# Performance work log

Hardware: AMD Instinct MI355X
Metric: run time of the kernel (lower is better)

Reference implementation:

```python
import jax, jax.numpy as jnp
import numpy as np

N = 100000   # nodes
DIM = 128    # feature dim
E = 800000   # edges per hop
K = 4        # hops
BN_EPS = 1e-5


def setup_inputs() -> dict:
    key = jax.random.key(0)
    ks = jax.random.split(key, 24)
    inp = {}
    for i in range(K):
        inp[f"x{i}"] = jax.random.normal(ks[i], (N, DIM), dtype=jnp.float32)
    inp["edge_attr"] = jax.random.normal(ks[4], (E, DIM), dtype=jnp.float32)
    for i in range(K):
        inp[f"e{i}"] = jax.random.randint(ks[5 + i], (2, E), 0, N, dtype=jnp.int32)
    s1 = 1.0 / np.sqrt(DIM)
    s2 = 1.0 / np.sqrt(2 * DIM)
    inp["W1"] = jax.random.uniform(ks[9], (DIM, 2 * DIM), jnp.float32, -s1, s1)
    inp["b1"] = jax.random.uniform(ks[10], (2 * DIM,), jnp.float32, -s1, s1)
    inp["bn1_g"] = jnp.ones((2 * DIM,), jnp.float32)
    inp["bn1_b"] = jnp.zeros((2 * DIM,), jnp.float32)
    inp["W2"] = jax.random.uniform(ks[11], (2 * DIM, DIM), jnp.float32, -s2, s2)
    inp["b2"] = jax.random.uniform(ks[12], (DIM,), jnp.float32, -s2, s2)
    inp["bn2_g"] = jnp.ones((DIM,), jnp.float32)
    inp["bn2_b"] = jnp.zeros((DIM,), jnp.float32)
    inp["bn3_g"] = jnp.ones((DIM,), jnp.float32)
    inp["bn3_b"] = jnp.zeros((DIM,), jnp.float32)
    inp["eps_param"] = jnp.zeros((K + 1, DIM), jnp.float32)  # nn.Parameter(zeros)
    return inp


def _bn(h, g, b):
    # BatchNorm1d, train-mode math: batch mean / biased var per feature
    m = jnp.mean(h, axis=0)
    v = jnp.var(h, axis=0)
    return g * (h - m) * jax.lax.rsqrt(v + BN_EPS) + b


def _propagate(x, edge_index, edge_attr):
    # message: relu(x_j [+ edge_attr]); aggregate: scatter-add at dst
    msg = x[edge_index[0]]                      # [E, DIM] gather from src
    if edge_attr is not None:
        msg = msg + edge_attr
    msg = jax.nn.relu(msg)
    return jax.ops.segment_sum(msg, edge_index[1], num_segments=N)


def reference(x0, x1, x2, x3, edge_attr, e0, e1, e2, e3,
              W1, b1, bn1_g, bn1_b, W2, b2, bn2_g, bn2_b,
              bn3_g, bn3_b, eps_param):
    xs = [x0, x1, x2, x3]
    es = [e0, e1, e2, e3]
    result = (1.0 + eps_param[0]) * x0
    for i in range(K):
        ea = edge_attr if i == 0 else None
        result = result + (1.0 + eps_param[i + 1]) * _propagate(xs[i], es[i], ea)
    # GIN MLP: Linear -> BN -> ReLU -> Linear -> BN -> ReLU
    h = jax.nn.relu(_bn(result @ W1 + b1, bn1_g, bn1_b))
    h = jax.nn.relu(_bn(h @ W2 + b2, bn2_g, bn2_b))
    # outer ConvBlock: BN -> act (relu, not last layer); dropout in eval = identity
    h = jax.nn.relu(_bn(h, bn3_g, bn3_b))
    return h  # new x[0]; original also carries XX through unchanged
```

## Files before the change

kernel.cpp:

```cpp
#include <hip/hip_runtime.h>
#include <cstdint>
#include <cstddef>

#define NN 100000
#define D 128
#define NE 800000
#define BN_EPS 1e-5f

#define M4 (4 * NN)
#define CH 1000
#define NB 400
#define GB 782

typedef __attribute__((ext_vector_type(4))) float f32x4;
typedef __attribute__((ext_vector_type(2))) float f32x2;
typedef __attribute__((ext_vector_type(8))) short s16x8;

__device__ inline unsigned short f2bf(float f) {
  unsigned int u = __builtin_bit_cast(unsigned int, f);
  u += 0x7FFFu + ((u >> 16) & 1u);
  return (unsigned short)(u >> 16);
}
__device__ inline float bf2f(unsigned short u) {
  unsigned int x = ((unsigned int)u) << 16;
  return __builtin_bit_cast(float, x);
}
__device__ inline f32x2 ntload2(const float* p) {
  return __builtin_nontemporal_load(reinterpret_cast<const f32x2*>(p));
}

__global__ __launch_bounds__(256) void k_prep(const float* __restrict__ W1,
                                              const float* __restrict__ W2,
                                              unsigned short* __restrict__ W1T,
                                              unsigned short* __restrict__ W2T) {
  int i = blockIdx.x * 256 + threadIdx.x;
  if (i >= 32768) return;
  int k1 = i >> 8, n1 = i & 255;
  W1T[n1 * 128 + k1] = f2bf(W1[i]);
  int k2 = i >> 7, n2 = i & 127;
  W2T[n2 * 256 + k2] = f2bf(W2[i]);
}

__global__ __launch_bounds__(256) void k_count(
    const int* __restrict__ e0, const int* __restrict__ e1,
    const int* __restrict__ e2, const int* __restrict__ e3,
    unsigned int* __restrict__ pcount, unsigned char* __restrict__ wrank) {
  const int h = blockIdx.y;
  const int* e = h == 0 ? e0 : h == 1 ? e1 : h == 2 ? e2 : e3;
  const int eid = blockIdx.x * 256 + threadIdx.x;
  const int dst = e[NE + eid];
  unsigned int old = atomicAdd(&pcount[dst], 1u << (8 * h));
  wrank[h * NE + eid] = (unsigned char)((old >> (8 * h)) & 0xFFu);
}

__global__ __launch_bounds__(256) void k_scanA(const unsigned int* __restrict__ pcount,
                                               int* __restrict__ bsum) {
  __shared__ int red[256];
  const int b = blockIdx.x, t = threadIdx.x;
  int s = 0;
  if (t < 250) {
    unsigned int p = pcount[b * 250 + t];
    s = (int)((p & 0xFFu) + ((p >> 8) & 0xFFu) + ((p >> 16) & 0xFFu) + (p >> 24));
  }
  red[t] = s; __syncthreads();
  for (int off = 128; off > 0; off >>= 1) {
    if (t < off) red[t] += red[t + off];
    __syncthreads();
  }
  if (t == 0) bsum[b] = red[0];
}

__global__ __launch_bounds__(512) void k_scanB(const int* __restrict__ bsum,
                                               int* __restrict__ bpre) {
  __shared__ int s[512];
  const int t = threadIdx.x;
  const int v = (t < NB) ? bsum[t] : 0;
  s[t] = v; __syncthreads();
  for (int off = 1; off < 512; off <<= 1) {
    int x = s[t];
    if (t >= off) x += s[t - off];
    __syncthreads(); s[t] = x; __syncthreads();
  }
  if (t < NB) bpre[t] = s[t] - v;
}

__global__ __launch_bounds__(256) void k_scanC(const unsigned int* __restrict__ pcount,
                                               const int* __restrict__ bpre,
                                               int* __restrict__ offsets) {
  __shared__ int cnt[CH];
  __shared__ int part[256];
  const int b = blockIdx.x, t = threadIdx.x;
  if (t < 250) {
    unsigned int p = pcount[b * 250 + t];
    cnt[t * 4 + 0] = (int)(p & 0xFFu);
    cnt[t * 4 + 1] = (int)((p >> 8) & 0xFFu);
    cnt[t * 4 + 2] = (int)((p >> 16) & 0xFFu);
    cnt[t * 4 + 3] = (int)(p >> 24);
  }
  __syncthreads();
  int own = 0;
#pragma unroll
  for (int j = 0; j < 4; j++) {
    int idx = t * 4 + j;
    if (idx < CH) own += cnt[idx];
  }
  part[t] = own; __syncthreads();
  for (int off = 1; off < 256; off <<= 1) {
    int x = part[t];
    if (t >= off) x += part[t - off];
    __syncthreads(); part[t] = x; __syncthreads();
  }
  int run = bpre[b] + part[t] - own;
#pragma unroll
  for (int j = 0; j < 4; j++) {
    int idx = t * 4 + j;
    if (idx < CH) { offsets[b * CH + idx] = run; run += cnt[idx]; }
  }
  if (b == 0 && t == 0) offsets[M4] = 4 * NE;
}

__global__ __launch_bounds__(256) void k_place(
    const int* __restrict__ e0, const int* __restrict__ e1,
    const int* __restrict__ e2, const int* __restrict__ e3,
    const int* __restrict__ offsets, const unsigned char* __restrict__ wrank,
    int* __restrict__ srcs, int* __restrict__ eids) {
  const int h = blockIdx.y;
  const int* e = h == 0 ? e0 : h == 1 ? e1 : h == 2 ? e2 : e3;
  const int eid = blockIdx.x * 256 + threadIdx.x;
  const int dst = e[NE + eid];
  const int pos = offsets[dst * 4 + h] + (int)wrank[h * NE + eid];
  if (h == 0) {
    eids[pos] = eid;
  } else {
    srcs[pos] = e[eid];
  }
}

__global__ __launch_bounds__(256) void k_gather(
    const float* __restrict__ x0, const float* __restrict__ x1,
    const float* __restrict__ x2, const float* __restrict__ x3,
    const float* __restrict__ edge_attr, const float* __restrict__ eps,
    const int* __restrict__ e0, const int* __restrict__ offsets,
    const int* __restrict__ srcs, const int* __restrict__ eids,
    unsigned short* __restrict__ result) {
  const int dst  = blockIdx.x * 4 + (threadIdx.x >> 6);
  const int lane = threadIdx.x & 63;
  const int d    = lane * 2;

  const int4 ob = *reinterpret_cast<const int4*>(offsets + 4 * dst);
  const int o0 = ob.x, b1 = ob.y, b2 = ob.z, b3 = ob.w;
  const int o4 = offsets[4 * dst + 4];

  float2 h0 = make_float2(0.f, 0.f);
  float2 h1 = make_float2(0.f, 0.f);
  float2 h2 = make_float2(0.f, 0.f);
  float2 h3 = make_float2(0.f, 0.f);

  {
    int j = o0;
    for (; j + 4 <= b1; j += 4) {
      const int q0 = eids[j], q1 = eids[j + 1], q2 = eids[j + 2], q3 = eids[j + 3];
      const int p0 = e0[q0], p1 = e0[q1], p2 = e0[q2], p3 = e0[q3];
      f32x2 w0 = ntload2(edge_attr + (size_t)q0 * D + d);
      f32x2 w1 = ntload2(edge_attr + (size_t)q1 * D + d);
      f32x2 w2 = ntload2(edge_attr + (size_t)q2 * D + d);
      f32x2 w3 = ntload2(edge_attr + (size_t)q3 * D + d);
      float2 v0 = *reinterpret_cast<const float2*>(x0 + p0 * D + d);
      float2 v1 = *reinterpret_cast<const float2*>(x0 + p1 * D + d);
      float2 v2 = *reinterpret_cast<const float2*>(x0 + p2 * D + d);
      float2 v3 = *reinterpret_cast<const float2*>(x0 + p3 * D + d);
      h0.x += fmaxf(v0.x + w0[0], 0.f); h0.y += fmaxf(v0.y + w0[1], 0.f);
      h0.x += fmaxf(v1.x + w1[0], 0.f); h0.y += fmaxf(v1.y + w1[1], 0.f);
      h0.x += fmaxf(v2.x + w2[0], 0.f); h0.y += fmaxf(v2.y + w2[1], 0.f);
      h0.x += fmaxf(v3.x + w3[0], 0.f); h0.y += fmaxf(v3.y + w3[1], 0.f);
    }
    for (; j < b1; ++j) {
      const int q = eids[j];
      const int p = e0[q];
      f32x2 w = ntload2(edge_attr + (size_t)q * D + d);
      float2 v = *reinterpret_cast<const float2*>(x0 + p * D + d);
      h0.x += fmaxf(v.x + w[0], 0.f); h0.y += fmaxf(v.y + w[1], 0.f);
    }
  }

#define HOP_LOOP(XP, ACC, BEG, END) do {                                       \
    int j_ = (BEG);                                                            \
    for (; j_ + 4 <= (END); j_ += 4) {                                         \
      const int p0_ = srcs[j_], p1_ = srcs[j_ + 1];                            \
      const int p2_ = srcs[j_ + 2], p3_ = srcs[j_ + 3];                        \
      float2 v0_ = *reinterpret_cast<const float2*>((XP) + p0_ * D + d);       \
      float2 v1_ = *reinterpret_cast<const float2*>((XP) + p1_ * D + d);       \
      float2 v2_ = *reinterpret_cast<const float2*>((XP) + p2_ * D + d);       \
      float2 v3_ = *reinterpret_cast<const float2*>((XP) + p3_ * D + d);       \
      ACC.x += fmaxf(v0_.x, 0.f); ACC.y += fmaxf(v0_.y, 0.f);                  \
      ACC.x += fmaxf(v1_.x, 0.f); ACC.y += fmaxf(v1_.y, 0.f);                  \
      ACC.x += fmaxf(v2_.x, 0.f); ACC.y += fmaxf(v2_.y, 0.f);                  \
      ACC.x += fmaxf(v3_.x, 0.f); ACC.y += fmaxf(v3_.y, 0.f);                  \
    }                                                                          \
    for (; j_ < (END); ++j_) {                                                 \
      const int p_ = srcs[j_];                                                 \
      float2 v_ = *reinterpret_cast<const float2*>((XP) + p_ * D + d);         \
      ACC.x += fmaxf(v_.x, 0.f); ACC.y += fmaxf(v_.y, 0.f);                    \
    }                                                                          \
  } while (0)

  HOP_LOOP(x1, h1, b1, b2);
  HOP_LOOP(x2, h2, b2, b3);
  HOP_LOOP(x3, h3, b3, o4);
#undef HOP_LOOP

  float2 e0v = *reinterpret_cast<const float2*>(eps + d);
  float2 s1 = *reinterpret_cast<const float2*>(eps + 1 * D + d);
  float2 s2 = *reinterpret_cast<const float2*>(eps + 2 * D + d);
  float2 s3 = *reinterpret_cast<const float2*>(eps + 3 * D + d);
  float2 s4 = *reinterpret_cast<const float2*>(eps + 4 * D + d);
  float2 xv = *reinterpret_cast<const float2*>(x0 + dst * D + d);

  float ax = (1.f + e0v.x) * xv.x + (1.f + s1.x) * h0.x + (1.f + s2.x) * h1.x
           + (1.f + s3.x) * h2.x + (1.f + s4.x) * h3.x;
  float ay = (1.f + e0v.y) * xv.y + (1.f + s1.y) * h0.y + (1.f + s2.y) * h1.y
           + (1.f + s3.y) * h2.y + (1.f + s4.y) * h3.y;

  reinterpret_cast<unsigned int*>(result)[dst * 64 + lane] =
      (unsigned int)f2bf(ax) | ((unsigned int)f2bf(ay) << 16);
}

__global__ __launch_bounds__(512) void k_gemm1(const unsigned short* __restrict__ Ab,
                                               const unsigned short* __restrict__ W1T,
                                               unsigned short* __restrict__ t1b,
                                               float* __restrict__ sums1,
                                               float* __restrict__ sumsq1) {
  __shared__ float ls[256], lq[256];
  const int tid = threadIdx.x;
  if (tid < 256) { ls[tid] = 0.f; lq[tid] = 0.f; }
  __syncthreads();

  const int lane = tid & 63, wave = tid >> 6;
  const int ln = lane & 15, lk = lane >> 4;
  const int m0 = blockIdx.x * 128 + wave * 16;
  const int arow = m0 + ln;
  const bool av = arow < NN;

  f32x4 acc[16];
#pragma unroll
  for (int t = 0; t < 16; t++) acc[t] = (f32x4)0.f;

#pragma unroll
  for (int kk = 0; kk < 4; kk++) {
    const int kb = kk * 32 + lk * 8;
    s16x8 a = (s16x8)(short)0;
    if (av) a = *reinterpret_cast<const s16x8*>(Ab + arow * 128 + kb);
#pragma unroll
    for (int t = 0; t < 16; t++) {
      s16x8 b = *reinterpret_cast<const s16x8*>(W1T + (t * 16 + ln) * 128 + kb);
      acc[t] = __builtin_amdgcn_mfma_f32_16x16x32_bf16(a, b, acc[t], 0, 0, 0);
    }
  }
#pragma unroll
  for (int t = 0; t < 16; t++) {
    float cs = 0.f, cq = 0.f;
#pragma unroll
    for (int r = 0; r < 4; r++) {
      const int row = m0 + lk * 4 + r;
      float v = acc[t][r];
      if (row < NN) t1b[(size_t)row * 256 + t * 16 + ln] = f2bf(v);
      cs += v;
      cq = fmaf(v, v, cq);
    }
    atomicAdd(&ls[t * 16 + ln], cs);
    atomicAdd(&lq[t * 16 + ln], cq);
  }
  __syncthreads();
  if (tid < 256) {
    unsafeAtomicAdd(&sums1[tid], ls[tid]);
    unsafeAtomicAdd(&sumsq1[tid], lq[tid]);
  }
}

__global__ __launch_bounds__(512) void k_gemm2(const unsigned short* __restrict__ t1b,
                                               const unsigned short* __restrict__ W2T,
                                               const float* __restrict__ sums1,
                                               const float* __restrict__ sumsq1,
                                               const float* __restrict__ bn1_g,
                                               const float* __restrict__ bn1_b,
                                               float* __restrict__ C,
                                               float* __restrict__ sums2,
                                               float* __restrict__ sumsq2) {
  __shared__ float s1s[256], s1h[256];
  __shared__ float ls[128], lq[128];
  const int tid = threadIdx.x;
  if (tid < 256) {
    float mean = sums1[tid] * (1.f / NN);
    float var  = sumsq1[tid] * (1.f / NN) - mean * mean;
    float rs   = rsqrtf(var + BN_EPS);
    float s    = bn1_g[tid] * rs;
    s1s[tid] = s;
    s1h[tid] = bn1_b[tid] - mean * s;
  }
  if (tid < 128) { ls[tid] = 0.f; lq[tid] = 0.f; }
  __syncthreads();

  const int lane = tid & 63, wave = tid >> 6;
  const int ln = lane & 15, lk = lane >> 4;
  const int m0 = blockIdx.x * 128 + wave * 16;
  const int arow = m0 + ln;
  const bool av = arow < NN;

  f32x4 acc[8];
#pragma unroll
  for (int t = 0; t < 8; t++) acc[t] = (f32x4)0.f;

#pragma unroll
  for (int kk = 0; kk < 8; kk++) {
    const int kb = kk * 32 + lk * 8;
    s16x8 raw = (s16x8)(short)0;
    if (av) raw = *reinterpret_cast<const s16x8*>(t1b + (size_t)arow * 256 + kb);
    s16x8 a;
#pragma unroll
    for (int i = 0; i < 8; i++) {
      const int col = kb + i;
      float v = fmaxf(fmaf(s1s[col], bf2f((unsigned short)raw[i]), s1h[col]), 0.f);
      a[i] = (short)f2bf(av ? v : 0.f);
    }
#pragma unroll
    for (int t = 0; t < 8; t++) {
      s16x8 b = *reinterpret_cast<const s16x8*>(W2T + (t * 16 + ln) * 256 + kb);
      acc[t] = __builtin_amdgcn_mfma_f32_16x16x32_bf16(a, b, acc[t], 0, 0, 0);
    }
  }
#pragma unroll
  for (int t = 0; t < 8; t++) {
    float cs = 0.f, cq = 0.f;
#pragma unroll
    for (int r = 0; r < 4; r++) {
      const int row = m0 + lk * 4 + r;
      float v = acc[t][r];
      if (row < NN) {
        C[(size_t)row * 128 + t * 16 + ln] = v;
        cs += v;
        cq = fmaf(v, v, cq);
      }
    }
    atomicAdd(&ls[t * 16 + ln], cs);
    atomicAdd(&lq[t * 16 + ln], cq);
  }
  __syncthreads();
  if (tid < 128) {
    unsafeAtomicAdd(&sums2[tid], ls[tid]);
    unsafeAtomicAdd(&sumsq2[tid], lq[tid]);
  }
}

__global__ __launch_bounds__(256) void k_colstats3(const float* __restrict__ X,
                                                   const float* __restrict__ sums2,
                                                   const float* __restrict__ sumsq2,
                                                   const float* __restrict__ bn2_g,
                                                   const float* __restrict__ bn2_b,
                                                   float* __restrict__ sums3,
                                                   float* __restrict__ sumsq3) {
  const long total = (long)NN * 128;
  const long stride = (long)gridDim.x * 256;
  const long start = (long)blockIdx.x * 256 + threadIdx.x;
  const int c = (int)(start & 127);
  float mean = sums2[c] * (1.f / NN);
  float var  = sumsq2[c] * (1.f / NN) - mean * mean;
  float rs   = rsqrtf(var + BN_EPS);
  float scale = bn2_g[c] * rs;
  float shiftv = bn2_b[c] - mean * scale;
  float s = 0.f, q = 0.f;
  for (long idx = start; idx < total; idx += stride) {
    float v = fmaxf(fmaf(scale, X[idx], shiftv), 0.f);
    s += v;
    q = fmaf(v, v, q);
  }
  unsafeAtomicAdd(&sums3[c], s);
  unsafeAtomicAdd(&sumsq3[c], q);
}

__global__ __launch_bounds__(256) void k_final(float* __restrict__ t2,
                                               const float* __restrict__ sums2,
                                               const float* __restrict__ sumsq2,
                                               const float* __restrict__ bn2_g,
                                               const float* __restrict__ bn2_b,
                                               const float* __restrict__ sums3,
                                               const float* __restrict__ sumsq3,
                                               const float* __restrict__ bn3_g,
                                               const float* __restrict__ bn3_b) {
  int i4 = blockIdx.x * 256 + threadIdx.x;
  if (i4 >= NN * D / 4) return;
  int d = (i4 & 31) * 4;
  float4 v = reinterpret_cast<float4*>(t2)[i4];
  float o[4];
  float* vv = reinterpret_cast<float*>(&v);
#pragma unroll
  for (int j = 0; j < 4; j++) {
    int c = d + j;
    float m2 = sums2[c] * (1.f / NN);
    float va2 = sumsq2[c] * (1.f / NN) - m2 * m2;
    float r2 = rsqrtf(va2 + BN_EPS);
    float a2 = bn2_g[c] * r2;
    float h2 = bn2_b[c] - m2 * a2;
    float m3 = sums3[c] * (1.f / NN);
    float va3 = sumsq3[c] * (1.f / NN) - m3 * m3;
    float r3 = rsqrtf(va3 + BN_EPS);
    float a3 = bn3_g[c] * r3;
    float h3 = bn3_b[c] - m3 * a3;
    o[j] = fmaxf(fmaf(a3, fmaxf(fmaf(a2, vv[j], h2), 0.f), h3), 0.f);
  }
  reinterpret_cast<float4*>(t2)[i4] = make_float4(o[0], o[1], o[2], o[3]);
}

extern "C" void kernel_launch(void* const* d_in, const int* in_sizes, int n_in,
                              void* d_out, int out_size, void* d_ws, size_t ws_size,
                              hipStream_t stream) {
  const float* x0 = (const float*)d_in[0];
  const float* x1 = (const float*)d_in[1];
  const float* x2 = (const float*)d_in[2];
  const float* x3 = (const float*)d_in[3];
  const float* edge_attr = (const float*)d_in[4];
  const int* e0 = (const int*)d_in[5];
  const int* e1 = (const int*)d_in[6];
  const int* e2 = (const int*)d_in[7];
  const int* e3 = (const int*)d_in[8];
  const float* W1 = (const float*)d_in[9];
  const float* bn1_g = (const float*)d_in[11];
  const float* bn1_b = (const float*)d_in[12];
  const float* W2 = (const float*)d_in[13];
  const float* bn2_g = (const float*)d_in[15];
  const float* bn2_b = (const float*)d_in[16];
  const float* bn3_g = (const float*)d_in[17];
  const float* bn3_b = (const float*)d_in[18];
  const float* eps = (const float*)d_in[19];

  char* ws = (char*)d_ws;
  unsigned short* resultb = (unsigned short*)ws;
  unsigned short* t1b = (unsigned short*)(ws + (size_t)NN * D * 2);
  float* stats = (float*)(ws + (size_t)NN * D * 2 + (size_t)NN * 256 * 2);
  float* sums1  = stats;
  float* sumsq1 = sums1 + 256;
  float* sums2  = sumsq1 + 256;
  float* sumsq2 = sums2 + 128;
  float* sums3  = sumsq2 + 128;
  float* sumsq3 = sums3 + 128;
  unsigned short* W1T = (unsigned short*)(sumsq3 + 128);
  unsigned short* W2T = W1T + 32768;
  unsigned int* pcount = (unsigned int*)(W2T + 32768);
  unsigned char* wrank = (unsigned char*)(pcount + NN);

  int* offsets = (int*)t1b;
  int* bsum    = offsets + M4 + 1;
  int* bpre    = bsum + NB;
  int* srcs    = bpre + NB;
  int* eids    = srcs + 4 * NE;

  float* t2 = (float*)d_out;

  hipMemsetAsync(pcount, 0, NN * sizeof(unsigned int), stream);
  hipMemsetAsync(stats, 0, 1024 * sizeof(float), stream);

  k_prep<<<128, 256, 0, stream>>>(W1, W2, W1T, W2T);

  k_count<<<dim3(NE / 256, 4), 256, 0, stream>>>(e0, e1, e2, e3, pcount, wrank);
  k_scanA<<<NB, 256, 0, stream>>>(pcount, bsum);
  k_scanB<<<1, 512, 0, stream>>>(bsum, bpre);
  k_scanC<<<NB, 256, 0, stream>>>(pcount, bpre, offsets);
  k_place<<<dim3(NE / 256, 4), 256, 0, stream>>>(e0, e1, e2, e3, offsets, wrank, srcs, eids);

  k_gather<<<NN / 4, 256, 0, stream>>>(x0, x1, x2, x3, edge_attr, eps, e0,
                                       offsets, srcs, eids, resultb);

  k_gemm1<<<GB, 512, 0, stream>>>(resultb, W1T, t1b, sums1, sumsq1);
  k_gemm2<<<GB, 512, 0, stream>>>(t1b, W2T, sums1, sumsq1, bn1_g, bn1_b,
                                  t2, sums2, sumsq2);
  k_colstats3<<<512, 256, 0, stream>>>(t2, sums2, sumsq2, bn2_g, bn2_b, sums3, sumsq3);
  k_final<<<NN * D / 4 / 256, 256, 0, stream>>>(t2, sums2, sumsq2, bn2_g, bn2_b,
                                                sums3, sumsq3, bn3_g, bn3_b);
}
```

Before: 861.7 us.

## Gather from bf16 copies of node features and store GEMM2 output in bf16

Adds a pre-pass that converts the four node-feature tables to bf16 so that the random gathers in the aggregation kernel read half as many bytes. The hop-0 edge list now stores (src, eid) pairs, which removes the dependent e0[eid] lookup. The GEMM2 output is written as bf16 into workspace and read by the column-stats and final BN kernels, which write fp32 into the output buffer. The conversion pass adds a full read and write of all four tables, and the bf16 rounding of inputs and intermediates loses precision.

After: 899.6 us. +4.4%, slower.

```diff
diff --git a/kernel.cpp b/kernel.cpp
--- a/kernel.cpp
+++ b/kernel.cpp
@@ -25,8 +25,28 @@
   unsigned int x = ((unsigned int)u) << 16;
   return __builtin_bit_cast(float, x);
 }
+__device__ inline float2 bfpair(unsigned int w) {
+  return make_float2(__builtin_bit_cast(float, w << 16),
+                     __builtin_bit_cast(float, w & 0xFFFF0000u));
+}
 __device__ inline f32x2 ntload2(const float* p) {
   return __builtin_nontemporal_load(reinterpret_cast<const f32x2*>(p));
+}
+
+__global__ __launch_bounds__(256) void k_xbf(const float* __restrict__ x0,
+                                             const float* __restrict__ x1,
+                                             const float* __restrict__ x2,
+                                             const float* __restrict__ x3,
+                                             unsigned short* __restrict__ xb01,
+                                             unsigned short* __restrict__ xb23) {
+  const int tbl = blockIdx.y;
+  const float* x = tbl == 0 ? x0 : tbl == 1 ? x1 : tbl == 2 ? x2 : x3;
+  unsigned short* o = (tbl < 2 ? xb01 : xb23) + (size_t)(tbl & 1) * NN * D;
+  int i4 = blockIdx.x * 256 + threadIdx.x;
+  float4 v = reinterpret_cast<const float4*>(x)[i4];
+  ushort4 u;
+  u.x = f2bf(v.x); u.y = f2bf(v.y); u.z = f2bf(v.z); u.w = f2bf(v.w);
+  reinterpret_cast<ushort4*>(o)[i4] = u;
 }
 
 __global__ __launch_bounds__(256) void k_prep(const float* __restrict__ W1,
@@ -123,26 +143,30 @@
     const int* __restrict__ e0, const int* __restrict__ e1,
     const int* __restrict__ e2, const int* __restrict__ e3,
     const int* __restrict__ offsets, const unsigned char* __restrict__ wrank,
-    int* __restrict__ srcs, int* __restrict__ eids) {
+    int* __restrict__ srcs, int2* __restrict__ pair0) {
   const int h = blockIdx.y;
   const int* e = h == 0 ? e0 : h == 1 ? e1 : h == 2 ? e2 : e3;
   const int eid = blockIdx.x * 256 + threadIdx.x;
+  const int src = e[eid];
   const int dst = e[NE + eid];
   const int pos = offsets[dst * 4 + h] + (int)wrank[h * NE + eid];
   if (h == 0) {
-    eids[pos] = eid;
+    pair0[pos] = make_int2(src, eid);
   } else {
-    srcs[pos] = e[eid];
+    srcs[pos] = src;
   }
 }
 
 __global__ __launch_bounds__(256) void k_gather(
-    const float* __restrict__ x0, const float* __restrict__ x1,
-    const float* __restrict__ x2, const float* __restrict__ x3,
+    const unsigned short* __restrict__ xb01, const unsigned short* __restrict__ xb23,
     const float* __restrict__ edge_attr, const float* __restrict__ eps,
-    const int* __restrict__ e0, const int* __restrict__ offsets,
-    const int* __restrict__ srcs, const int* __restrict__ eids,
-    unsigned short* __restrict__ result) {
+    const int* __restrict__ offsets, const int* __restrict__ srcs,
+    const int2* __restrict__ pair0, unsigned short* __restrict__ result) {
+  const unsigned short* xb0 = xb01;
+  const unsigned short* xb1 = xb01 + (size_t)NN * D;
+  const unsigned short* xb2 = xb23;
+  const unsigned short* xb3 = xb23 + (size_t)NN * D;
+
   const int dst  = blockIdx.x * 4 + (threadIdx.x >> 6);
   const int lane = threadIdx.x & 63;
   const int d    = lane * 2;
@@ -159,26 +183,27 @@
   {
     int j = o0;
     for (; j + 4 <= b1; j += 4) {
-      const int q0 = eids[j], q1 = eids[j + 1], q2 = eids[j + 2], q3 = eids[j + 3];
-      const int p0 = e0[q0], p1 = e0[q1], p2 = e0[q2], p3 = e0[q3];
-      f32x2 w0 = ntload2(edge_attr + (size_t)q0 * D + d);
-      f32x2 w1 = ntload2(edge_attr + (size_t)q1 * D + d);
-      f32x2 w2 = ntload2(edge_attr + (size_t)q2 * D + d);
-      f32x2 w3 = ntload2(edge_attr + (size_t)q3 * D + d);
-      float2 v0 = *reinterpret_cast<const float2*>(x0 + p0 * D + d);
-      float2 v1 = *reinterpret_cast<const float2*>(x0 + p1 * D + d);
-      float2 v2 = *reinterpret_cast<const float2*>(x0 + p2 * D + d);
-      float2 v3 = *reinterpret_cast<const float2*>(x0 + p3 * D + d);
+      const int2 pq0 = pair0[j],     pq1 = pair0[j + 1];
+      const int2 pq2 = pair0[j + 2], pq3 = pair0[j + 3];
+      unsigned int a0 = *reinterpret_cast<const unsigned int*>(xb0 + pq0.x * D + d);
+      unsigned int a1 = *reinterpret_cast<const unsigned int*>(xb0 + pq1.x * D + d);
+      unsigned int a2 = *reinterpret_cast<const unsigned int*>(xb0 + pq2.x * D + d);
+      unsigned int a3 = *reinterpret_cast<const unsigned int*>(xb0 + pq3.x * D + d);
+      f32x2 w0 = ntload2(edge_attr + (size_t)pq0.y * D + d);
+      f32x2 w1 = ntload2(edge_attr + (size_t)pq1.y * D + d);
+      f32x2 w2 = ntload2(edge_attr + (size_t)pq2.y * D + d);
+      f32x2 w3 = ntload2(edge_attr + (size_t)pq3.y * D + d);
+      float2 v0 = bfpair(a0), v1 = bfpair(a1), v2 = bfpair(a2), v3 = bfpair(a3);
       h0.x += fmaxf(v0.x + w0[0], 0.f); h0.y += fmaxf(v0.y + w0[1], 0.f);
       h0.x += fmaxf(v1.x + w1[0], 0.f); h0.y += fmaxf(v1.y + w1[1], 0.f);
       h0.x += fmaxf(v2.x + w2[0], 0.f); h0.y += fmaxf(v2.y + w2[1], 0.f);
       h0.x += fmaxf(v3.x + w3[0], 0.f); h0.y += fmaxf(v3.y + w3[1], 0.f);
     }
     for (; j < b1; ++j) {
-      const int q = eids[j];
-      const int p = e0[q];
-      f32x2 w = ntload2(edge_attr + (size_t)q * D + d);
-      float2 v = *reinterpret_cast<const float2*>(x0 + p * D + d);
+      const int2 pq = pair0[j];
+      unsigned int a = *reinterpret_cast<const unsigned int*>(xb0 + pq.x * D + d);
+      f32x2 w = ntload2(edge_attr + (size_t)pq.y * D + d);
+      float2 v = bfpair(a);
       h0.x += fmaxf(v.x + w[0], 0.f); h0.y += fmaxf(v.y + w[1], 0.f);
     }
   }
@@ -188,10 +213,12 @@
     for (; j_ + 4 <= (END); j_ += 4) {                                         \
       const int p0_ = srcs[j_], p1_ = srcs[j_ + 1];                            \
       const int p2_ = srcs[j_ + 2], p3_ = srcs[j_ + 3];                        \
-      float2 v0_ = *reinterpret_cast<const float2*>((XP) + p0_ * D + d);       \
-      float2 v1_ = *reinterpret_cast<const float2*>((XP) + p1_ * D + d);       \
-      float2 v2_ = *reinterpret_cast<const float2*>((XP) + p2_ * D + d);       \
-      float2 v3_ = *reinterpret_cast<const float2*>((XP) + p3_ * D + d);       \
+      unsigned int a0_ = *reinterpret_cast<const unsigned int*>((XP) + p0_ * D + d); \
+      unsigned int a1_ = *reinterpret_cast<const unsigned int*>((XP) + p1_ * D + d); \
+      unsigned int a2_ = *reinterpret_cast<const unsigned int*>((XP) + p2_ * D + d); \
+      unsigned int a3_ = *reinterpret_cast<const unsigned int*>((XP) + p3_ * D + d); \
+      float2 v0_ = bfpair(a0_), v1_ = bfpair(a1_);                             \
+      float2 v2_ = bfpair(a2_), v3_ = bfpair(a3_);                             \
       ACC.x += fmaxf(v0_.x, 0.f); ACC.y += fmaxf(v0_.y, 0.f);                  \
       ACC.x += fmaxf(v1_.x, 0.f); ACC.y += fmaxf(v1_.y, 0.f);                  \
       ACC.x += fmaxf(v2_.x, 0.f); ACC.y += fmaxf(v2_.y, 0.f);                  \
@@ -199,14 +226,15 @@
     }                                                                          \
     for (; j_ < (END); ++j_) {                                                 \
       const int p_ = srcs[j_];                                                 \
-      float2 v_ = *reinterpret_cast<const float2*>((XP) + p_ * D + d);         \
+      unsigned int a_ = *reinterpret_cast<const unsigned int*>((XP) + p_ * D + d); \
+      float2 v_ = bfpair(a_);                                                  \
       ACC.x += fmaxf(v_.x, 0.f); ACC.y += fmaxf(v_.y, 0.f);                    \
     }                                                                          \
   } while (0)
 
-  HOP_LOOP(x1, h1, b1, b2);
-  HOP_LOOP(x2, h2, b2, b3);
-  HOP_LOOP(x3, h3, b3, o4);
+  HOP_LOOP(xb1, h1, b1, b2);
+  HOP_LOOP(xb2, h2, b2, b3);
+  HOP_LOOP(xb3, h3, b3, o4);
 #undef HOP_LOOP
 
   float2 e0v = *reinterpret_cast<const float2*>(eps + d);
@@ -214,7 +242,7 @@
   float2 s2 = *reinterpret_cast<const float2*>(eps + 2 * D + d);
   float2 s3 = *reinterpret_cast<const float2*>(eps + 3 * D + d);
   float2 s4 = *reinterpret_cast<const float2*>(eps + 4 * D + d);
-  float2 xv = *reinterpret_cast<const float2*>(x0 + dst * D + d);
+  float2 xv = bfpair(*reinterpret_cast<const unsigned int*>(xb0 + dst * D + d));
 
   float ax = (1.f + e0v.x) * xv.x + (1.f + s1.x) * h0.x + (1.f + s2.x) * h1.x
            + (1.f + s3.x) * h2.x + (1.f + s4.x) * h3.x;
@@ -283,7 +311,7 @@
                                                const float* __restrict__ sumsq1,
                                                const float* __restrict__ bn1_g,
                                                const float* __restrict__ bn1_b,
-                                               float* __restrict__ C,
+                                               unsigned short* __restrict__ t2b,
                                                float* __restrict__ sums2,
                                                float* __restrict__ sumsq2) {
   __shared__ float s1s[256], s1h[256];
@@ -336,7 +364,7 @@
       const int row = m0 + lk * 4 + r;
       float v = acc[t][r];
       if (row < NN) {
-        C[(size_t)row * 128 + t * 16 + ln] = v;
+        t2b[(size_t)row * 128 + t * 16 + ln] = f2bf(v);
         cs += v;
         cq = fmaf(v, v, cq);
       }
@@ -351,33 +379,41 @@
   }
 }
 
-__global__ __launch_bounds__(256) void k_colstats3(const float* __restrict__ X,
+__global__ __launch_bounds__(256) void k_colstats3(const unsigned short* __restrict__ X,
                                                    const float* __restrict__ sums2,
                                                    const float* __restrict__ sumsq2,
                                                    const float* __restrict__ bn2_g,
                                                    const float* __restrict__ bn2_b,
                                                    float* __restrict__ sums3,
                                                    float* __restrict__ sumsq3) {
-  const long total = (long)NN * 128;
+  const long total = (long)NN * 64;
   const long stride = (long)gridDim.x * 256;
   const long start = (long)blockIdx.x * 256 + threadIdx.x;
-  const int c = (int)(start & 127);
-  float mean = sums2[c] * (1.f / NN);
-  float var  = sumsq2[c] * (1.f / NN) - mean * mean;
-  float rs   = rsqrtf(var + BN_EPS);
-  float scale = bn2_g[c] * rs;
-  float shiftv = bn2_b[c] - mean * scale;
-  float s = 0.f, q = 0.f;
+  const int c = (int)(start & 63) * 2;
+  float m2a = sums2[c] * (1.f / NN),   m2b = sums2[c + 1] * (1.f / NN);
+  float va  = sumsq2[c] * (1.f / NN) - m2a * m2a;
+  float vb  = sumsq2[c + 1] * (1.f / NN) - m2b * m2b;
+  float sa = bn2_g[c] * rsqrtf(va + BN_EPS);
+  float sb = bn2_g[c + 1] * rsqrtf(vb + BN_EPS);
+  float ha = bn2_b[c] - m2a * sa;
+  float hb = bn2_b[c + 1] - m2b * sb;
+  float s0 = 0.f, q0 = 0.f, s1 = 0.f, q1 = 0.f;
+  const unsigned int* Xu = reinterpret_cast<const unsigned int*>(X);
   for (long idx = start; idx < total; idx += stride) {
-    float v = fmaxf(fmaf(scale, X[idx], shiftv), 0.f);
-    s += v;
-    q = fmaf(v, v, q);
-  }
-  unsafeAtomicAdd(&sums3[c], s);
-  unsafeAtomicAdd(&sumsq3[c], q);
-}
-
-__global__ __launch_bounds__(256) void k_final(float* __restrict__ t2,
+    float2 v = bfpair(Xu[idx]);
+    float a = fmaxf(fmaf(sa, v.x, ha), 0.f);
+    float b = fmaxf(fmaf(sb, v.y, hb), 0.f);
+    s0 += a; q0 = fmaf(a, a, q0);
+    s1 += b; q1 = fmaf(b, b, q1);
+  }
+  unsafeAtomicAdd(&sums3[c], s0);
+  unsafeAtomicAdd(&sumsq3[c], q0);
+  unsafeAtomicAdd(&sums3[c + 1], s1);
+  unsafeAtomicAdd(&sumsq3[c + 1], q1);
+}
+
+__global__ __launch_bounds__(256) void k_final(const unsigned short* __restrict__ t2b,
+                                               float* __restrict__ out,
                                                const float* __restrict__ sums2,
                                                const float* __restrict__ sumsq2,
                                                const float* __restrict__ bn2_g,
@@ -386,28 +422,25 @@
                                                const float* __restrict__ sumsq3,
                                                const float* __restrict__ bn3_g,
                                                const float* __restrict__ bn3_b) {
-  int i4 = blockIdx.x * 256 + threadIdx.x;
-  if (i4 >= NN * D / 4) return;
-  int d = (i4 & 31) * 4;
-  float4 v = reinterpret_cast<float4*>(t2)[i4];
-  float o[4];
-  float* vv = reinterpret_cast<float*>(&v);
-#pragma unroll
-  for (int j = 0; j < 4; j++) {
-    int c = d + j;
-    float m2 = sums2[c] * (1.f / NN);
-    float va2 = sumsq2[c] * (1.f / NN) - m2 * m2;
-    float r2 = rsqrtf(va2 + BN_EPS);
-    float a2 = bn2_g[c] * r2;
-    float h2 = bn2_b[c] - m2 * a2;
-    float m3 = sums3[c] * (1.f / NN);
-    float va3 = sumsq3[c] * (1.f / NN) - m3 * m3;
-    float r3 = rsqrtf(va3 + BN_EPS);
-    float a3 = bn3_g[c] * r3;
-    float h3 = bn3_b[c] - m3 * a3;
-    o[j] = fmaxf(fmaf(a3, fmaxf(fmaf(a2, vv[j], h2), 0.f), h3), 0.f);
-  }
-  reinterpret_cast<float4*>(t2)[i4] = make_float4(o[0], o[1], o[2], o[3]);
+  int i2 = blockIdx.x * 256 + threadIdx.x;
+  int c = (i2 & 63) * 2;
+  float2 v = bfpair(reinterpret_cast<const unsigned int*>(t2b)[i2]);
+  float o[2];
+#pragma unroll
+  for (int j = 0; j < 2; j++) {
+    int cc = c + j;
+    float vv = j ? v.y : v.x;
+    float m2 = sums2[cc] * (1.f / NN);
+    float va2 = sumsq2[cc] * (1.f / NN) - m2 * m2;
+    float a2 = bn2_g[cc] * rsqrtf(va2 + BN_EPS);
+    float h2 = bn2_b[cc] - m2 * a2;
+    float m3 = sums3[cc] * (1.f / NN);
+    float va3 = sumsq3[cc] * (1.f / NN) - m3 * m3;
+    float a3 = bn3_g[cc] * rsqrtf(va3 + BN_EPS);
+    float h3 = bn3_b[cc] - m3 * a3;
+    o[j] = fmaxf(fmaf(a3, fmaxf(fmaf(a2, vv, h2), 0.f), h3), 0.f);
+  }
+  *reinterpret_cast<float2*>(out + (size_t)i2 * 2) = make_float2(o[0], o[1]);
 }
 
 extern "C" void kernel_launch(void* const* d_in, const int* in_sizes, int n_in,
@@ -434,6 +467,7 @@
 
   char* ws = (char*)d_ws;
   unsigned short* resultb = (unsigned short*)ws;
+  unsigned short* t2b = resultb;
   unsigned short* t1b = (unsigned short*)(ws + (size_t)NN * D * 2);
   float* stats = (float*)(ws + (size_t)NN * D * 2 + (size_t)NN * 256 * 2);
   float* sums1  = stats;
@@ -446,33 +480,34 @@
   unsigned short* W2T = W1T + 32768;
   unsigned int* pcount = (unsigned int*)(W2T + 32768);
   unsigned char* wrank = (unsigned char*)(pcount + NN);
+  unsigned short* xb23 = (unsigned short*)(wrank + 4 * NE);
+  unsigned short* xb01 = (unsigned short*)d_out;
 
   int* offsets = (int*)t1b;
   int* bsum    = offsets + M4 + 1;
   int* bpre    = bsum + NB;
   int* srcs    = bpre + NB;
-  int* eids    = srcs + 4 * NE;
-
-  float* t2 = (float*)d_out;
+  int2* pair0  = (int2*)(srcs + 4 * NE);
 
   hipMemsetAsync(pcount, 0, NN * sizeof(unsigned int), stream);
   hipMemsetAsync(stats, 0, 1024 * sizeof(float), stream);
 
+  k_xbf<<<dim3(12500, 4), 256, 0, stream>>>(x0, x1, x2, x3, xb01, xb23);
   k_prep<<<128, 256, 0, stream>>>(W1, W2, W1T, W2T);
 
   k_count<<<dim3(NE / 256, 4), 256, 0, stream>>>(e0, e1, e2, e3, pcount, wrank);
   k_scanA<<<NB, 256, 0, stream>>>(pcount, bsum);
   k_scanB<<<1, 512, 0, stream>>>(bsum, bpre);
   k_scanC<<<NB, 256, 0, stream>>>(pcount, bpre, offsets);
-  k_place<<<dim3(NE / 256, 4), 256, 0, stream>>>(e0, e1, e2, e3, offsets, wrank, srcs, eids);
-
-  k_gather<<<NN / 4, 256, 0, stream>>>(x0, x1, x2, x3, edge_attr, eps, e0,
-                                       offsets, srcs, eids, resultb);
+  k_place<<<dim3(NE / 256, 4), 256, 0, stream>>>(e0, e1, e2, e3, offsets, wrank, srcs, pair0);
+
+  k_gather<<<NN / 4, 256, 0, stream>>>(xb01, xb23, edge_attr, eps,
+                                       offsets, srcs, pair0, resultb);
 
   k_gemm1<<<GB, 512, 0, stream>>>(resultb, W1T, t1b, sums1, sumsq1);
   k_gemm2<<<GB, 512, 0, stream>>>(t1b, W2T, sums1, sumsq1, bn1_g, bn1_b,
-                                  t2, sums2, sumsq2);
-  k_colstats3<<<512, 256, 0, stream>>>(t2, sums2, sumsq2, bn2_g, bn2_b, sums3, sumsq3);
-  k_final<<<NN * D / 4 / 256, 256, 0, stream>>>(t2, sums2, sumsq2, bn2_g, bn2_b,
-                                                sums3, sumsq3, bn3_g, bn3_b);
-}
+                                  t2b, sums2, sumsq2);
+  k_colstats3<<<512, 256, 0, stream>>>(t2b, sums2, sumsq2, bn2_g, bn2_b, sums3, sumsq3);
+  k_final<<<25000, 256, 0, stream>>>(t2b, (float*)d_out, sums2, sumsq2, bn2_g, bn2_b,
+                                     sums3, sumsq3, bn3_g, bn3_b);
+}
```
